# Optimization experiments

Hardware: AMD Instinct MI355X
Metric: run time of the kernel (lower is better)

## Reference

```python
import jax, jax.numpy as jnp
import numpy as np
from jax import lax

MAX_FEATURES = 50000
WIDTH = 256
EMBED = 2 * WIDTH
NUM_CLASS = 2
BATCH = 64
SEQ = 512


def setup_inputs() -> dict:
    key = jax.random.key(0)
    ks = jax.random.split(key, 10)
    s = lambda *shape: 1.0 / np.sqrt(shape[0])
    tokens = jax.random.randint(ks[0], (BATCH, SEQ), 0, MAX_FEATURES, dtype=jnp.int32)
    emb = jax.random.normal(ks[1], (MAX_FEATURES, EMBED), jnp.float32) * 0.05
    W1 = jax.random.normal(ks[2], (EMBED, WIDTH), jnp.float32) * s(EMBED)
    U1 = jax.random.normal(ks[3], (WIDTH, WIDTH), jnp.float32) * s(WIDTH)
    b1 = jnp.zeros((WIDTH,), jnp.float32)
    W2 = jax.random.normal(ks[4], (WIDTH, WIDTH), jnp.float32) * s(WIDTH)
    U2 = jax.random.normal(ks[5], (WIDTH, WIDTH), jnp.float32) * s(WIDTH)
    b2 = jnp.zeros((WIDTH,), jnp.float32)
    Wd = jax.random.normal(ks[6], (WIDTH, NUM_CLASS), jnp.float32) * s(WIDTH)
    bd = jnp.zeros((NUM_CLASS,), jnp.float32)
    return {"tokens": tokens, "emb": emb, "W1": W1, "U1": U1, "b1": b1,
            "W2": W2, "U2": U2, "b2": b2, "Wd": Wd, "bd": bd}


def _simple_rnn(x, W, U, b, return_sequences):
    # x: [B, S, D] -> precompute input projection once (big GEMM), then scan
    B = x.shape[0]
    H = U.shape[0]
    xw = jnp.einsum('bsd,dh->bsh', x, W) + b  # [B, S, H]
    def step(h, xt):
        h_new = jnp.tanh(xt + h @ U)
        return h_new, h_new
    h0 = jnp.zeros((B, H), x.dtype)
    h_last, hs = lax.scan(step, h0, jnp.swapaxes(xw, 0, 1))  # hs: [S, B, H]
    if return_sequences:
        return jnp.swapaxes(hs, 0, 1)  # [B, S, H]
    return h_last  # [B, H]


def reference(tokens, emb, W1, U1, b1, W2, U2, b2, Wd, bd):
    x = emb[tokens]                                  # [B, S, 2W] embedding lookup
    h1 = _simple_rnn(x, W1, U1, b1, return_sequences=True)   # [B, S, W]
    h2 = _simple_rnn(h1, W2, U2, b2, return_sequences=False)  # [B, W]
    logits = h2 @ Wd + bd                            # [B, num_class]
    return jax.nn.softmax(logits, axis=-1)
```

## Files before the change

### kernel.cpp

```cpp
#include <hip/hip_runtime.h>

typedef __attribute__((ext_vector_type(8))) short bf16x8;
typedef __attribute__((ext_vector_type(4))) float f32x4;

static __device__ __forceinline__ unsigned short f2bf(float x) {
    unsigned int u = __float_as_uint(x);
    u += 0x7fffu + ((u >> 16) & 1u);
    return (unsigned short)(u >> 16);
}

static __device__ __forceinline__ void barrier_lds_only() {
    __asm__ volatile("s_waitcnt lgkmcnt(0)\n\ts_barrier" ::: "memory");
}

__global__ void transpose4(const float* __restrict__ s0, const float* __restrict__ s1,
                           const float* __restrict__ s2, const float* __restrict__ s3,
                           unsigned short* __restrict__ d0, unsigned short* __restrict__ d1,
                           unsigned short* __restrict__ d2, unsigned short* __restrict__ d3) {
    int which = blockIdx.y;
    const float* src = which == 0 ? s0 : which == 1 ? s1 : which == 2 ? s2 : s3;
    unsigned short* dst = which == 0 ? d0 : which == 1 ? d1 : which == 2 ? d2 : d3;
    int K = (which == 0) ? 512 : 256;
    int idx = blockIdx.x * 256 + threadIdx.x;
    if (idx >= K * 256) return;
    int k = idx >> 8;
    int n = idx & 255;
    dst[n * K + k] = f2bf(src[idx]);
}

template<bool GATHER>
__global__ __launch_bounds__(256, 4) void gemm_mfma(
    const void* __restrict__ Aptr, const int* __restrict__ tokens,
    const unsigned short* __restrict__ Bt, const float* __restrict__ bias,
    float* __restrict__ C, int M, int N, int K)
{
    const int bn0 = blockIdx.x * 64;
    const int m0  = blockIdx.y * 64;
    const int tid = threadIdx.x;

    __shared__ unsigned short As[64 * 40];
    __shared__ unsigned short Bs[64 * 40];
    __shared__ int tok[64];

    if (GATHER) {
        if (tid < 64) tok[tid] = tokens[m0 + tid];
        __syncthreads();
    }

    const int r  = tid >> 2;
    const int c0 = (tid & 3) * 8;
    const int w  = tid >> 6;
    const int L  = tid & 63;
    const int ml = L & 15;
    const int q  = L >> 4;
    const int kq = q * 8;

    f32x4 acc[4] = {};

    for (int k0 = 0; k0 < K; k0 += 32) {
        unsigned short tmp[8];
        if (GATHER) {
            const float* src = (const float*)Aptr + (size_t)tok[r] * K + k0 + c0;
            float4 f0 = *(const float4*)(src);
            float4 f1 = *(const float4*)(src + 4);
            tmp[0]=f2bf(f0.x); tmp[1]=f2bf(f0.y); tmp[2]=f2bf(f0.z); tmp[3]=f2bf(f0.w);
            tmp[4]=f2bf(f1.x); tmp[5]=f2bf(f1.y); tmp[6]=f2bf(f1.z); tmp[7]=f2bf(f1.w);
        } else {
            const unsigned short* src = (const unsigned short*)Aptr + (size_t)(m0 + r) * K + k0 + c0;
            *(uint4*)tmp = *(const uint4*)src;
        }
        *(uint4*)&As[r * 40 + c0] = *(const uint4*)tmp;
        *(uint4*)&Bs[r * 40 + c0] = *(const uint4*)(Bt + (size_t)(bn0 + r) * K + k0 + c0);
        __syncthreads();

        bf16x8 av = *(const bf16x8*)&As[(16 * w + ml) * 40 + kq];
#pragma unroll
        for (int ns = 0; ns < 4; ++ns) {
            bf16x8 bv = *(const bf16x8*)&Bs[(ns * 16 + ml) * 40 + kq];
            acc[ns] = __builtin_amdgcn_mfma_f32_16x16x32_bf16(av, bv, acc[ns], 0, 0, 0);
        }
        __syncthreads();
    }

#pragma unroll
    for (int ns = 0; ns < 4; ++ns) {
        int gn = bn0 + ns * 16 + ml;
        float bv = bias[gn];
#pragma unroll
        for (int rr = 0; rr < 4; ++rr) {
            int gm = m0 + 16 * w + q * 4 + rr;
            C[(size_t)gm * N + gn] = acc[ns][rr] + bv;
        }
    }
}

template<bool SEQ>
__global__ __launch_bounds__(256, 1) void rnn_scan_mfma(
    const float* __restrict__ xw,
    const unsigned short* __restrict__ Ut,
    unsigned short* __restrict__ out_seq,
    float* __restrict__ out_last)
{
    const int b   = blockIdx.x;
    const int tid = threadIdx.x;
    const int w   = tid >> 6;
    const int L   = tid & 63;
    const int col = w * 64 + L;
    const int q   = L >> 4;
    const int ml  = L & 15;

    __shared__ unsigned short hsh[2][256];

    bf16x8 ufrag[4][8];
#pragma unroll
    for (int i = 0; i < 4; ++i) {
        const unsigned short* up = Ut + (size_t)((w * 4 + i) * 16 + ml) * 256 + q * 8;
#pragma unroll
        for (int kt = 0; kt < 8; ++kt)
            ufrag[i][kt] = *(const bf16x8*)(up + kt * 32);
    }

    hsh[0][tid] = 0;

    const float* xb = xw + (size_t)b * 512 * 256 + col;
    unsigned short* op = SEQ ? out_seq + (size_t)b * 512 * 256 + col : nullptr;

    float xq0 = xb[0 * 256];
    float xq1 = xb[1 * 256];
    float xq2 = xb[2 * 256];
    float xq3 = xb[3 * 256];
    const float* xpf = xb + 4 * 256;

    float lastv = 0.f;
    __syncthreads();

#define SCAN_STEP(CUR, XQ, PF)                                                       \
    {                                                                                \
        bf16x8 af[8];                                                                \
        _Pragma("unroll")                                                            \
        for (int kt = 0; kt < 8; ++kt)                                               \
            af[kt] = *(const bf16x8*)&hsh[CUR][kt * 32 + q * 8];                     \
        float xnew = 0.f;                                                            \
        if (PF) { xnew = *xpf; xpf += 256; }                                         \
        f32x4 accA[4] = {}, accB[4] = {};                                            \
        _Pragma("unroll")                                                            \
        for (int kt = 0; kt < 8; kt += 2) {                                          \
            _Pragma("unroll")                                                        \
            for (int i = 0; i < 4; ++i)                                              \
                accA[i] = __builtin_amdgcn_mfma_f32_16x16x32_bf16(af[kt], ufrag[i][kt], accA[i], 0, 0, 0);       \
            _Pragma("unroll")                                                        \
            for (int i = 0; i < 4; ++i)                                              \
                accB[i] = __builtin_amdgcn_mfma_f32_16x16x32_bf16(af[kt + 1], ufrag[i][kt + 1], accB[i], 0, 0, 0); \
        }                                                                            \
        float zA = (q == 0) ? accA[0][0] : (q == 1) ? accA[1][0] : (q == 2) ? accA[2][0] : accA[3][0]; \
        float zB = (q == 0) ? accB[0][0] : (q == 1) ? accB[1][0] : (q == 2) ? accB[2][0] : accB[3][0]; \
        float z  = zA + zB + XQ;                                                     \
        float e  = __expf(2.f * z);                  \
        float hn = 1.f - 2.f * __builtin_amdgcn_rcpf(e + 1.f);                       \
        lastv = hn;                                                                  \
        unsigned short hb = f2bf(hn);                                                \
        hsh[(CUR) ^ 1][col] = hb;                                                    \
        if (SEQ) { *op = hb; op += 256; }                                            \
        XQ = xnew;                                                                   \
        barrier_lds_only();                                                         \
    }

    for (int tt = 0; tt < 508; tt += 4) {
        SCAN_STEP(0, xq0, 1)
        SCAN_STEP(1, xq1, 1)
        SCAN_STEP(0, xq2, 1)
        SCAN_STEP(1, xq3, 1)
    }
    SCAN_STEP(0, xq0, 0)
    SCAN_STEP(1, xq1, 0)
    SCAN_STEP(0, xq2, 0)
    SCAN_STEP(1, xq3, 0)
#undef SCAN_STEP

    if (!SEQ) out_last[b * 256 + col] = lastv;
}

__global__ void head_kernel(const float* __restrict__ h2, const float* __restrict__ Wd,
                            const float* __restrict__ bd, float* __restrict__ out)
{
    int tid = threadIdx.x;
    int b = tid >> 1, c = tid & 1;
    float s = bd[c];
    for (int jj = 0; jj < 256; ++jj) s = fmaf(h2[b * 256 + jj], Wd[jj * 2 + c], s);
    __shared__ float lg[128];
    lg[tid] = s;
    __syncthreads();
    float o0 = lg[b * 2 + 0], o1 = lg[b * 2 + 1];
    float m = fmaxf(o0, o1);
    float z = __expf(o0 - m) + __expf(o1 - m);
    out[tid] = __expf(s - m) * __builtin_amdgcn_rcpf(z);
}

extern "C" void kernel_launch(void* const* d_in, const int* in_sizes, int n_in,
                              void* d_out, int out_size, void* d_ws, size_t ws_size,
                              hipStream_t stream) {
    const int*   tokens = (const int*)d_in[0];
    const float* emb    = (const float*)d_in[1];
    const float* W1     = (const float*)d_in[2];
    const float* U1     = (const float*)d_in[3];
    const float* b1     = (const float*)d_in[4];
    const float* W2     = (const float*)d_in[5];
    const float* U2     = (const float*)d_in[6];
    const float* b2     = (const float*)d_in[7];
    const float* Wd     = (const float*)d_in[8];
    const float* bd     = (const float*)d_in[9];
    float* out = (float*)d_out;

    char* ws = (char*)d_ws;
    float*          xw  = (float*)ws;
    unsigned short* h1  = (unsigned short*)(ws + (33554432));
    char*           p   = ws + 33554432 + 16777216;
    unsigned short* W1t = (unsigned short*)p;            p += 512 * 256 * 2;
    unsigned short* W2t = (unsigned short*)p;            p += 256 * 256 * 2;
    unsigned short* U1t = (unsigned short*)p;            p += 256 * 256 * 2;
    unsigned short* U2t = (unsigned short*)p;            p += 256 * 256 * 2;
    float*          h2  = (float*)p;

    const int M = 64 * 512;

    transpose4<<<dim3(512, 4), 256, 0, stream>>>(W1, W2, U1, U2, W1t, W2t, U1t, U2t);

    gemm_mfma<true><<<dim3(256 / 64, M / 64), 256, 0, stream>>>(
        emb, tokens, W1t, b1, xw, M, 256, 512);

    rnn_scan_mfma<true><<<64, 256, 0, stream>>>(xw, U1t, h1, nullptr);

    gemm_mfma<false><<<dim3(256 / 64, M / 64), 256, 0, stream>>>(
        h1, nullptr, W2t, b2, xw, M, 256, 256);

    rnn_scan_mfma<false><<<64, 256, 0, stream>>>(xw, U2t, nullptr, h2);

    head_kernel<<<1, 128, 0, stream>>>(h2, Wd, bd, out);
}
```

Baseline: 659.7 us.

## Fuse both RNN layers and second input projection into one pipelined scan kernel

Replaces the two sequential scan kernels and the middle GEMM with a single 768-thread kernel per batch row. Three warp groups play separate roles: the layer-1 recurrence, the W2 projection of h1, and the layer-2 recurrence. They are pipelined with a one-step skew through double-buffered LDS. This removes the h1 round trip through global memory, the second GEMM launch and one serial scan pass, so the two recurrences overlap in time. In exchange each block needs three times the threads and registers, the per-step work grows, and there are two extra pipeline ticks.

Result: slower. 679.2 us (+2.9%).

```diff
diff --git a/kernel.cpp b/kernel.cpp
--- a/kernel.cpp
+++ b/kernel.cpp
@@ -94,90 +94,113 @@
     }
 }
 
-template<bool SEQ>
-__global__ __launch_bounds__(256, 1) void rnn_scan_mfma(
+__global__ __launch_bounds__(768, 1) void rnn_fused(
     const float* __restrict__ xw,
-    const unsigned short* __restrict__ Ut,
-    unsigned short* __restrict__ out_seq,
+    const unsigned short* __restrict__ U1t,
+    const unsigned short* __restrict__ W2t,
+    const unsigned short* __restrict__ U2t,
+    const float* __restrict__ b2,
     float* __restrict__ out_last)
 {
-    const int b   = blockIdx.x;
-    const int tid = threadIdx.x;
-    const int w   = tid >> 6;
-    const int L   = tid & 63;
-    const int col = w * 64 + L;
-    const int q   = L >> 4;
-    const int ml  = L & 15;
-
-    __shared__ unsigned short hsh[2][256];
-
+    const int b    = blockIdx.x;
+    const int tid  = threadIdx.x;
+    const int w    = tid >> 6;
+    const int role = w >> 2;
+    const int sw   = w & 3;
+    const int L    = tid & 63;
+    const int col  = sw * 64 + L;
+    const int q    = L >> 4;
+    const int ml   = L & 15;
+
+    __shared__ unsigned short h1sh[2][256];
+    __shared__ unsigned short h2sh[2][256];
+    __shared__ float          psh[2][256];
+
+    const unsigned short* Bmat = (role == 0) ? U1t : (role == 1) ? W2t : U2t;
     bf16x8 ufrag[4][8];
 #pragma unroll
     for (int i = 0; i < 4; ++i) {
-        const unsigned short* up = Ut + (size_t)((w * 4 + i) * 16 + ml) * 256 + q * 8;
+        const unsigned short* up = Bmat + (size_t)((sw * 4 + i) * 16 + ml) * 256 + q * 8;
 #pragma unroll
         for (int kt = 0; kt < 8; ++kt)
             ufrag[i][kt] = *(const bf16x8*)(up + kt * 32);
     }
 
-    hsh[0][tid] = 0;
-
+    if (tid < 256) { h1sh[1][tid] = 0; h2sh[1][tid] = 0; }
+
+    float b2c = 0.f;
     const float* xb = xw + (size_t)b * 512 * 256 + col;
-    unsigned short* op = SEQ ? out_seq + (size_t)b * 512 * 256 + col : nullptr;
-
-    float xq0 = xb[0 * 256];
-    float xq1 = xb[1 * 256];
-    float xq2 = xb[2 * 256];
-    float xq3 = xb[3 * 256];
     const float* xpf = xb + 4 * 256;
+    float xq0 = 0.f, xq1 = 0.f, xq2 = 0.f, xq3 = 0.f;
+    if (role == 0) {
+        xq0 = xb[0 * 256]; xq1 = xb[1 * 256]; xq2 = xb[2 * 256]; xq3 = xb[3 * 256];
+    } else if (role == 2) {
+        b2c = b2[col];
+    }
 
     float lastv = 0.f;
     __syncthreads();
 
-#define SCAN_STEP(CUR, XQ, PF)                                                       \
+#define LADDER(SRCBUF, RP)                                                           \
+    bf16x8 af[8];                                                                    \
+    _Pragma("unroll")                                                                \
+    for (int kt = 0; kt < 8; ++kt)                                                   \
+        af[kt] = *(const bf16x8*)&SRCBUF[RP][kt * 32 + q * 8];                       \
+    f32x4 acc[4] = {};                                                               \
+    _Pragma("unroll")                                                                \
+    for (int kt = 0; kt < 8; ++kt) {                                                 \
+        _Pragma("unroll")                                                            \
+        for (int i = 0; i < 4; ++i)                                                  \
+            acc[i] = __builtin_amdgcn_mfma_f32_16x16x32_bf16(af[kt], ufrag[i][kt], acc[i], 0, 0, 0); \
+    }                                                                                \
+    float z = (q == 0) ? acc[0][0] : (q == 1) ? acc[1][0] : (q == 2) ? acc[2][0] : acc[3][0];
+
+#define TICK(RP, XQ, PF, DO_A, DO_B, DO_C)                                           \
     {                                                                                \
-        bf16x8 af[8];                                                                \
-        _Pragma("unroll")                                                            \
-        for (int kt = 0; kt < 8; ++kt)                                               \
-            af[kt] = *(const bf16x8*)&hsh[CUR][kt * 32 + q * 8];                     \
-        float xnew = 0.f;                                                            \
-        if (PF) { xnew = *xpf; xpf += 256; }                                         \
-        f32x4 accA[4] = {}, accB[4] = {};                                            \
-        _Pragma("unroll")                                                            \
-        for (int kt = 0; kt < 8; kt += 2) {                                          \
-            _Pragma("unroll")                                                        \
-            for (int i = 0; i < 4; ++i)                                              \
-                accA[i] = __builtin_amdgcn_mfma_f32_16x16x32_bf16(af[kt], ufrag[i][kt], accA[i], 0, 0, 0);       \
-            _Pragma("unroll")                                                        \
-            for (int i = 0; i < 4; ++i)                                              \
-                accB[i] = __builtin_amdgcn_mfma_f32_16x16x32_bf16(af[kt + 1], ufrag[i][kt + 1], accB[i], 0, 0, 0); \
+        if (DO_A && role == 0) {                                                     \
+            float xnew = 0.f;                                                        \
+            if (PF) { xnew = *xpf; xpf += 256; }                                     \
+            LADDER(h1sh, RP)                                                         \
+            z += XQ;                                                                 \
+            float e  = __expf(2.f * z);              \
+            float hn = 1.f - 2.f * __builtin_amdgcn_rcpf(e + 1.f);                   \
+            h1sh[(RP) ^ 1][col] = f2bf(hn);                                          \
+            XQ = xnew;                                                               \
+        } else if (DO_B && role == 1) {                                              \
+            LADDER(h1sh, RP)                                                         \
+            psh[(RP) ^ 1][col] = z;                                                  \
+        } else if (DO_C && role == 2) {                                              \
+            float pv = psh[RP][col] + b2c;                                           \
+            LADDER(h2sh, RP)                                                         \
+            z += pv;                                                                 \
+            float e  = __expf(2.f * z);                                              \
+            float hn = 1.f - 2.f * __builtin_amdgcn_rcpf(e + 1.f);                   \
+            lastv = hn;                                                              \
+            h2sh[(RP) ^ 1][col] = f2bf(hn);                                          \
         }                                                                            \
-        float zA = (q == 0) ? accA[0][0] : (q == 1) ? accA[1][0] : (q == 2) ? accA[2][0] : accA[3][0]; \
-        float zB = (q == 0) ? accB[0][0] : (q == 1) ? accB[1][0] : (q == 2) ? accB[2][0] : accB[3][0]; \
-        float z  = zA + zB + XQ;                                                     \
-        float e  = __expf(2.f * z);                  \
-        float hn = 1.f - 2.f * __builtin_amdgcn_rcpf(e + 1.f);                       \
-        lastv = hn;                                                                  \
-        unsigned short hb = f2bf(hn);                                                \
-        hsh[(CUR) ^ 1][col] = hb;                                                    \
-        if (SEQ) { *op = hb; op += 256; }                                            \
-        XQ = xnew;                                                                   \
-        barrier_lds_only();                                                         \
-    }
-
-    for (int tt = 0; tt < 508; tt += 4) {
-        SCAN_STEP(0, xq0, 1)
-        SCAN_STEP(1, xq1, 1)
-        SCAN_STEP(0, xq2, 1)
-        SCAN_STEP(1, xq3, 1)
-    }
-    SCAN_STEP(0, xq0, 0)
-    SCAN_STEP(1, xq1, 0)
-    SCAN_STEP(0, xq2, 0)
-    SCAN_STEP(1, xq3, 0)
-#undef SCAN_STEP
-
-    if (!SEQ) out_last[b * 256 + col] = lastv;
+        barrier_lds_only();                                                          \
+    }
+
+    TICK(1, xq0, 1, 1, 1, 0)
+    TICK(0, xq1, 1, 1, 1, 0)
+    TICK(1, xq2, 1, 1, 1, 1)
+    TICK(0, xq3, 1, 1, 1, 1)
+    for (int tt = 4; tt < 508; tt += 4) {
+        TICK(1, xq0, 1, 1, 1, 1)
+        TICK(0, xq1, 1, 1, 1, 1)
+        TICK(1, xq2, 1, 1, 1, 1)
+        TICK(0, xq3, 1, 1, 1, 1)
+    }
+    TICK(1, xq0, 0, 1, 1, 1)
+    TICK(0, xq1, 0, 1, 1, 1)
+    TICK(1, xq2, 0, 1, 1, 1)
+    TICK(0, xq3, 0, 1, 1, 1)
+    TICK(1, xq0, 0, 0, 1, 1)
+    TICK(0, xq0, 0, 0, 0, 1)
+#undef TICK
+#undef LADDER
+
+    if (role == 2) out_last[b * 256 + col] = lastv;
 }
 
 __global__ void head_kernel(const float* __restrict__ h2, const float* __restrict__ Wd,
@@ -213,7 +236,6 @@
 
     char* ws = (char*)d_ws;
     float*          xw  = (float*)ws;
-    unsigned short* h1  = (unsigned short*)(ws + (33554432));
     char*           p   = ws + 33554432 + 16777216;
     unsigned short* W1t = (unsigned short*)p;            p += 512 * 256 * 2;
     unsigned short* W2t = (unsigned short*)p;            p += 256 * 256 * 2;
@@ -228,12 +250,7 @@
     gemm_mfma<true><<<dim3(256 / 64, M / 64), 256, 0, stream>>>(
         emb, tokens, W1t, b1, xw, M, 256, 512);
 
-    rnn_scan_mfma<true><<<64, 256, 0, stream>>>(xw, U1t, h1, nullptr);
-
-    gemm_mfma<false><<<dim3(256 / 64, M / 64), 256, 0, stream>>>(
-        h1, nullptr, W2t, b2, xw, M, 256, 256);
-
-    rnn_scan_mfma<false><<<64, 256, 0, stream>>>(xw, U2t, nullptr, h2);
+    rnn_fused<<<64, 768, 0, stream>>>(xw, U1t, W2t, U2t, b2, h2);
 
     head_kernel<<<1, 128, 0, stream>>>(h2, Wd, bd, out);
 }
```

## Fuse layer-2 input projection into layer-1 scan, drop intermediate h1 GEMM

Applied to the files above, without the earlier changes.

The first recurrent scan now also keeps W2 fragments in registers and multiplies each step's previous hidden state by W2. It writes the layer-2 pre-activation (plus b2) in place into the xw buffer one step behind, so the bf16 h1 sequence is never stored and the separate layer-2 GEMM launch is removed. The MFMA chains are also split into more independent accumulators to shorten dependency latency. This doubles the MFMA work and register pressure on the serial critical path of the first scan, in exchange for removing a full GEMM and its memory traffic.

New measurement: 983.2 us. 49.0% more time.

```diff
diff --git a/kernel.cpp b/kernel.cpp
--- a/kernel.cpp
+++ b/kernel.cpp
@@ -94,90 +94,194 @@
     }
 }
 
-template<bool SEQ>
-__global__ __launch_bounds__(256, 1) void rnn_scan_mfma(
+__global__ __launch_bounds__(256, 1) void rnn_scan_fused(
+    float* __restrict__ xw,
+    const unsigned short* __restrict__ U1t,
+    const unsigned short* __restrict__ W2t,
+    const float* __restrict__ b2)
+{
+    const int b   = blockIdx.x;
+    const int tid = threadIdx.x;
+    const int w   = tid >> 6;
+    const int L   = tid & 63;
+    const int col = tid;
+    const int q   = L >> 4;
+    const int ml  = L & 15;
+
+    __shared__ unsigned short hsh[2][256];
+
+    bf16x8 U1f[4][8], W2f[4][8];
+#pragma unroll
+    for (int i = 0; i < 4; ++i) {
+        const unsigned short* u1 = U1t + (size_t)((w * 4 + i) * 16 + ml) * 256 + q * 8;
+        const unsigned short* w2 = W2t + (size_t)((w * 4 + i) * 16 + ml) * 256 + q * 8;
+#pragma unroll
+        for (int kt = 0; kt < 8; ++kt) {
+            U1f[i][kt] = *(const bf16x8*)(u1 + kt * 32);
+            W2f[i][kt] = *(const bf16x8*)(w2 + kt * 32);
+        }
+    }
+
+    hsh[0][tid] = 0;
+    const float b2c = b2[col];
+    float* xb        = xw + (size_t)b * 512 * 256 + col;
+    const float* xpf = xb + 4 * 256;
+    float* pst       = xb - 256;
+    float xq0 = xb[0 * 256], xq1 = xb[1 * 256], xq2 = xb[2 * 256], xq3 = xb[3 * 256];
+    const f32x4 z4 = {0.f, 0.f, 0.f, 0.f};
+    __syncthreads();
+
+#define FTICK(RP, XQ, PF, ST)                                                        \
+    {                                                                                \
+        bf16x8 af[8];                                                                \
+        _Pragma("unroll")                                                            \
+        for (int kt = 0; kt < 8; ++kt)                                               \
+            af[kt] = *(const bf16x8*)&hsh[RP][kt * 32 + q * 8];                      \
+        float xnew = 0.f;                                                            \
+        if (PF) { xnew = *xpf; xpf += 256; }                                         \
+        f32x4 aU[4][4];                                                              \
+        f32x4 aW[4][2];                                                              \
+        _Pragma("unroll")                                                            \
+        for (int kt = 0; kt < 8; ++kt) {                                             \
+            _Pragma("unroll")                                                        \
+            for (int i = 0; i < 4; ++i)                                              \
+                aU[i][kt & 3] = __builtin_amdgcn_mfma_f32_16x16x32_bf16(             \
+                    af[kt], U1f[i][kt], (kt < 4) ? z4 : aU[i][kt & 3], 0, 0, 0);     \
+            _Pragma("unroll")                                                        \
+            for (int i = 0; i < 4; ++i)                                              \
+                aW[i][kt & 1] = __builtin_amdgcn_mfma_f32_16x16x32_bf16(             \
+                    af[kt], W2f[i][kt], (kt < 2) ? z4 : aW[i][kt & 1], 0, 0, 0);     \
+        }                                                                            \
+        float sU0 = aU[0][0][0] + aU[0][1][0] + aU[0][2][0] + aU[0][3][0];           \
+        float sU1 = aU[1][0][0] + aU[1][1][0] + aU[1][2][0] + aU[1][3][0];           \
+        float sU2 = aU[2][0][0] + aU[2][1][0] + aU[2][2][0] + aU[2][3][0];           \
+        float sU3 = aU[3][0][0] + aU[3][1][0] + aU[3][2][0] + aU[3][3][0];           \
+        float z = ((q == 0) ? sU0 : (q == 1) ? sU1 : (q == 2) ? sU2 : sU3) + XQ;     \
+        float e  = __expf(2.f * z);                  \
+        float hn = 1.f - 2.f * __builtin_amdgcn_rcpf(e + 1.f);                       \
+        hsh[(RP) ^ 1][col] = f2bf(hn);                                               \
+        if (ST) {                                                                    \
+            float sW0 = aW[0][0][0] + aW[0][1][0];                                   \
+            float sW1 = aW[1][0][0] + aW[1][1][0];                                   \
+            float sW2 = aW[2][0][0] + aW[2][1][0];                                   \
+            float sW3 = aW[3][0][0] + aW[3][1][0];                                   \
+            *pst = ((q == 0) ? sW0 : (q == 1) ? sW1 : (q == 2) ? sW2 : sW3) + b2c;   \
+        }                                                                            \
+        pst += 256;                                                                  \
+        XQ = xnew;                                                                   \
+        barrier_lds_only();                                                          \
+    }
+
+    FTICK(0, xq0, 1, 0)
+    FTICK(1, xq1, 1, 1)
+    FTICK(0, xq2, 1, 1)
+    FTICK(1, xq3, 1, 1)
+    for (int tt = 4; tt < 508; tt += 4) {
+        FTICK(0, xq0, 1, 1)
+        FTICK(1, xq1, 1, 1)
+        FTICK(0, xq2, 1, 1)
+        FTICK(1, xq3, 1, 1)
+    }
+    FTICK(0, xq0, 0, 1)
+    FTICK(1, xq1, 0, 1)
+    FTICK(0, xq2, 0, 1)
+    FTICK(1, xq3, 0, 1)
+#undef FTICK
+
+    {
+        bf16x8 af[8];
+#pragma unroll
+        for (int kt = 0; kt < 8; ++kt)
+            af[kt] = *(const bf16x8*)&hsh[0][kt * 32 + q * 8];
+        f32x4 aW[4][2];
+#pragma unroll
+        for (int kt = 0; kt < 8; ++kt)
+#pragma unroll
+            for (int i = 0; i < 4; ++i)
+                aW[i][kt & 1] = __builtin_amdgcn_mfma_f32_16x16x32_bf16(
+                    af[kt], W2f[i][kt], (kt < 2) ? z4 : aW[i][kt & 1], 0, 0, 0);
+        float sW0 = aW[0][0][0] + aW[0][1][0];
+        float sW1 = aW[1][0][0] + aW[1][1][0];
+        float sW2 = aW[2][0][0] + aW[2][1][0];
+        float sW3 = aW[3][0][0] + aW[3][1][0];
+        *pst = ((q == 0) ? sW0 : (q == 1) ? sW1 : (q == 2) ? sW2 : sW3) + b2c;
+    }
+}
+
+__global__ __launch_bounds__(256, 1) void rnn_scan2(
     const float* __restrict__ xw,
     const unsigned short* __restrict__ Ut,
-    unsigned short* __restrict__ out_seq,
     float* __restrict__ out_last)
 {
     const int b   = blockIdx.x;
     const int tid = threadIdx.x;
     const int w   = tid >> 6;
     const int L   = tid & 63;
-    const int col = w * 64 + L;
+    const int col = tid;
     const int q   = L >> 4;
     const int ml  = L & 15;
 
     __shared__ unsigned short hsh[2][256];
 
-    bf16x8 ufrag[4][8];
+    bf16x8 uf[4][8];
 #pragma unroll
     for (int i = 0; i < 4; ++i) {
         const unsigned short* up = Ut + (size_t)((w * 4 + i) * 16 + ml) * 256 + q * 8;
 #pragma unroll
         for (int kt = 0; kt < 8; ++kt)
-            ufrag[i][kt] = *(const bf16x8*)(up + kt * 32);
+            uf[kt == 0 ? i : i][kt] = *(const bf16x8*)(up + kt * 32);
     }
 
     hsh[0][tid] = 0;
-
-    const float* xb = xw + (size_t)b * 512 * 256 + col;
-    unsigned short* op = SEQ ? out_seq + (size_t)b * 512 * 256 + col : nullptr;
-
-    float xq0 = xb[0 * 256];
-    float xq1 = xb[1 * 256];
-    float xq2 = xb[2 * 256];
-    float xq3 = xb[3 * 256];
+    const float* xb  = xw + (size_t)b * 512 * 256 + col;
     const float* xpf = xb + 4 * 256;
-
+    float xq0 = xb[0 * 256], xq1 = xb[1 * 256], xq2 = xb[2 * 256], xq3 = xb[3 * 256];
+    const f32x4 z4 = {0.f, 0.f, 0.f, 0.f};
     float lastv = 0.f;
     __syncthreads();
 
-#define SCAN_STEP(CUR, XQ, PF)                                                       \
+#define STICK(RP, XQ, PF)                                                            \
     {                                                                                \
         bf16x8 af[8];                                                                \
         _Pragma("unroll")                                                            \
         for (int kt = 0; kt < 8; ++kt)                                               \
-            af[kt] = *(const bf16x8*)&hsh[CUR][kt * 32 + q * 8];                     \
+            af[kt] = *(const bf16x8*)&hsh[RP][kt * 32 + q * 8];                      \
         float xnew = 0.f;                                                            \
         if (PF) { xnew = *xpf; xpf += 256; }                                         \
-        f32x4 accA[4] = {}, accB[4] = {};                                            \
+        f32x4 aU[4][4];                                                              \
         _Pragma("unroll")                                                            \
-        for (int kt = 0; kt < 8; kt += 2) {                                          \
+        for (int kt = 0; kt < 8; ++kt) {                                             \
             _Pragma("unroll")                                                        \
             for (int i = 0; i < 4; ++i)                                              \
-                accA[i] = __builtin_amdgcn_mfma_f32_16x16x32_bf16(af[kt], ufrag[i][kt], accA[i], 0, 0, 0);       \
-            _Pragma("unroll")                                                        \
-            for (int i = 0; i < 4; ++i)                                              \
-                accB[i] = __builtin_amdgcn_mfma_f32_16x16x32_bf16(af[kt + 1], ufrag[i][kt + 1], accB[i], 0, 0, 0); \
+                aU[i][kt & 3] = __builtin_amdgcn_mfma_f32_16x16x32_bf16(             \
+                    af[kt], uf[i][kt], (kt < 4) ? z4 : aU[i][kt & 3], 0, 0, 0);      \
         }                                                                            \
-        float zA = (q == 0) ? accA[0][0] : (q == 1) ? accA[1][0] : (q == 2) ? accA[2][0] : accA[3][0]; \
-        float zB = (q == 0) ? accB[0][0] : (q == 1) ? accB[1][0] : (q == 2) ? accB[2][0] : accB[3][0]; \
-        float z  = zA + zB + XQ;                                                     \
-        float e  = __expf(2.f * z);                  \
+        float s0 = aU[0][0][0] + aU[0][1][0] + aU[0][2][0] + aU[0][3][0];            \
+        float s1 = aU[1][0][0] + aU[1][1][0] + aU[1][2][0] + aU[1][3][0];            \
+        float s2 = aU[2][0][0] + aU[2][1][0] + aU[2][2][0] + aU[2][3][0];            \
+        float s3 = aU[3][0][0] + aU[3][1][0] + aU[3][2][0] + aU[3][3][0];            \
+        float z = ((q == 0) ? s0 : (q == 1) ? s1 : (q == 2) ? s2 : s3) + XQ;         \
+        float e  = __expf(2.f * z);                                                  \
         float hn = 1.f - 2.f * __builtin_amdgcn_rcpf(e + 1.f);                       \
         lastv = hn;                                                                  \
-        unsigned short hb = f2bf(hn);                                                \
-        hsh[(CUR) ^ 1][col] = hb;                                                    \
-        if (SEQ) { *op = hb; op += 256; }                                            \
+        hsh[(RP) ^ 1][col] = f2bf(hn);                                               \
         XQ = xnew;                                                                   \
-        barrier_lds_only();                                                         \
+        barrier_lds_only();                                                          \
     }
 
     for (int tt = 0; tt < 508; tt += 4) {
-        SCAN_STEP(0, xq0, 1)
-        SCAN_STEP(1, xq1, 1)
-        SCAN_STEP(0, xq2, 1)
-        SCAN_STEP(1, xq3, 1)
-    }
-    SCAN_STEP(0, xq0, 0)
-    SCAN_STEP(1, xq1, 0)
-    SCAN_STEP(0, xq2, 0)
-    SCAN_STEP(1, xq3, 0)
-#undef SCAN_STEP
-
-    if (!SEQ) out_last[b * 256 + col] = lastv;
+        STICK(0, xq0, 1)
+        STICK(1, xq1, 1)
+        STICK(0, xq2, 1)
+        STICK(1, xq3, 1)
+    }
+    STICK(0, xq0, 0)
+    STICK(1, xq1, 0)
+    STICK(0, xq2, 0)
+    STICK(1, xq3, 0)
+#undef STICK
+
+    out_last[b * 256 + col] = lastv;
 }
 
 __global__ void head_kernel(const float* __restrict__ h2, const float* __restrict__ Wd,
@@ -213,7 +317,6 @@
 
     char* ws = (char*)d_ws;
     float*          xw  = (float*)ws;
-    unsigned short* h1  = (unsigned short*)(ws + (33554432));
     char*           p   = ws + 33554432 + 16777216;
     unsigned short* W1t = (unsigned short*)p;            p += 512 * 256 * 2;
     unsigned short* W2t = (unsigned short*)p;            p += 256 * 256 * 2;
@@ -228,12 +331,9 @@
     gemm_mfma<true><<<dim3(256 / 64, M / 64), 256, 0, stream>>>(
         emb, tokens, W1t, b1, xw, M, 256, 512);
 
-    rnn_scan_mfma<true><<<64, 256, 0, stream>>>(xw, U1t, h1, nullptr);
-
-    gemm_mfma<false><<<dim3(256 / 64, M / 64), 256, 0, stream>>>(
-        h1, nullptr, W2t, b2, xw, M, 256, 256);
-
-    rnn_scan_mfma<false><<<64, 256, 0, stream>>>(xw, U2t, nullptr, h2);
+    rnn_scan_fused<<<64, 256, 0, stream>>>(xw, U1t, W2t, b2);
+
+    rnn_scan2<<<64, 256, 0, stream>>>(xw, U2t, h2);
 
     head_kernel<<<1, 128, 0, stream>>>(h2, Wd, bd, out);
 }
```

## Pipeline both RNN layers in one kernel with flag-based producer-consumer sync

Applied to the files above, without the earlier changes.

Merges the layer-1 scan, the layer-2 input GEMM and the layer-2 scan into one 128-block kernel. Blocks 0-63 run layer 1 and publish h1 in chunks of 8 steps through release flags. Blocks 64-127 poll those flags and compute the W2 input projection inline alongside the U2 recurrence. This removes one scan launch and the separate GEMM, and overlaps the two sequential scans instead of running them back to back. In exchange it relies on all 128 blocks being co-resident, and the spin-wait uses a bounded timeout that silently breaks out, which could read stale h1 data.

Result: slower. 878.3 us (+33.1%).

```diff
diff --git a/kernel.cpp b/kernel.cpp
--- a/kernel.cpp
+++ b/kernel.cpp
@@ -7,6 +7,10 @@
     unsigned int u = __float_as_uint(x);
     u += 0x7fffu + ((u >> 16) & 1u);
     return (unsigned short)(u >> 16);
+}
+
+static __device__ __forceinline__ float selq(const f32x4* a, int q) {
+    return (q == 0) ? a[0][0] : (q == 1) ? a[1][0] : (q == 2) ? a[2][0] : a[3][0];
 }
 
 static __device__ __forceinline__ void barrier_lds_only() {
@@ -94,47 +98,47 @@
     }
 }
 
-template<bool SEQ>
-__global__ __launch_bounds__(256, 1) void rnn_scan_mfma(
+__global__ __launch_bounds__(256, 1) void rnn_pipe(
     const float* __restrict__ xw,
-    const unsigned short* __restrict__ Ut,
-    unsigned short* __restrict__ out_seq,
+    const unsigned short* __restrict__ U1t,
+    const unsigned short* __restrict__ W2t,
+    const unsigned short* __restrict__ U2t,
+    const float* __restrict__ b2,
+    unsigned short* h1g,
+    int* flags,
     float* __restrict__ out_last)
 {
-    const int b   = blockIdx.x;
+    const int bid = blockIdx.x;
     const int tid = threadIdx.x;
     const int w   = tid >> 6;
     const int L   = tid & 63;
-    const int col = w * 64 + L;
+    const int col = tid;
     const int q   = L >> 4;
     const int ml  = L & 15;
 
     __shared__ unsigned short hsh[2][256];
 
-    bf16x8 ufrag[4][8];
-#pragma unroll
-    for (int i = 0; i < 4; ++i) {
-        const unsigned short* up = Ut + (size_t)((w * 4 + i) * 16 + ml) * 256 + q * 8;
-#pragma unroll
-        for (int kt = 0; kt < 8; ++kt)
-            ufrag[i][kt] = *(const bf16x8*)(up + kt * 32);
-    }
-
-    hsh[0][tid] = 0;
-
-    const float* xb = xw + (size_t)b * 512 * 256 + col;
-    unsigned short* op = SEQ ? out_seq + (size_t)b * 512 * 256 + col : nullptr;
-
-    float xq0 = xb[0 * 256];
-    float xq1 = xb[1 * 256];
-    float xq2 = xb[2 * 256];
-    float xq3 = xb[3 * 256];
-    const float* xpf = xb + 4 * 256;
-
-    float lastv = 0.f;
-    __syncthreads();
-
-#define SCAN_STEP(CUR, XQ, PF)                                                       \
+    if (bid < 64) {
+        const int b = bid;
+        int* flagp = flags + b;
+
+        bf16x8 U1f[4][8];
+#pragma unroll
+        for (int i = 0; i < 4; ++i) {
+            const unsigned short* up = U1t + (size_t)((w * 4 + i) * 16 + ml) * 256 + q * 8;
+#pragma unroll
+            for (int kt = 0; kt < 8; ++kt)
+                U1f[i][kt] = *(const bf16x8*)(up + kt * 32);
+        }
+        hsh[0][tid] = 0;
+
+        const float* xb  = xw + (size_t)b * 512 * 256 + col;
+        const float* xpf = xb + 4 * 256;
+        unsigned short* op = h1g + (((size_t)b * 512) << 8) + col;
+        float xq0 = xb[0 * 256], xq1 = xb[1 * 256], xq2 = xb[2 * 256], xq3 = xb[3 * 256];
+        __syncthreads();
+
+#define PSTEP(CUR, XQ, PF)                                                           \
     {                                                                                \
         bf16x8 af[8];                                                                \
         _Pragma("unroll")                                                            \
@@ -147,37 +151,123 @@
         for (int kt = 0; kt < 8; kt += 2) {                                          \
             _Pragma("unroll")                                                        \
             for (int i = 0; i < 4; ++i)                                              \
-                accA[i] = __builtin_amdgcn_mfma_f32_16x16x32_bf16(af[kt], ufrag[i][kt], accA[i], 0, 0, 0);       \
-            _Pragma("unroll")                                                        \
-            for (int i = 0; i < 4; ++i)                                              \
-                accB[i] = __builtin_amdgcn_mfma_f32_16x16x32_bf16(af[kt + 1], ufrag[i][kt + 1], accB[i], 0, 0, 0); \
+                accA[i] = __builtin_amdgcn_mfma_f32_16x16x32_bf16(af[kt], U1f[i][kt], accA[i], 0, 0, 0);       \
+            _Pragma("unroll")                                                        \
+            for (int i = 0; i < 4; ++i)                                              \
+                accB[i] = __builtin_amdgcn_mfma_f32_16x16x32_bf16(af[kt + 1], U1f[i][kt + 1], accB[i], 0, 0, 0); \
         }                                                                            \
-        float zA = (q == 0) ? accA[0][0] : (q == 1) ? accA[1][0] : (q == 2) ? accA[2][0] : accA[3][0]; \
-        float zB = (q == 0) ? accB[0][0] : (q == 1) ? accB[1][0] : (q == 2) ? accB[2][0] : accB[3][0]; \
-        float z  = zA + zB + XQ;                                                     \
+        float z  = selq(accA, q) + selq(accB, q) + XQ;                               \
         float e  = __expf(2.f * z);                  \
         float hn = 1.f - 2.f * __builtin_amdgcn_rcpf(e + 1.f);                       \
-        lastv = hn;                                                                  \
         unsigned short hb = f2bf(hn);                                                \
         hsh[(CUR) ^ 1][col] = hb;                                                    \
-        if (SEQ) { *op = hb; op += 256; }                                            \
+        *op = hb; op += 256;                                                         \
         XQ = xnew;                                                                   \
-        barrier_lds_only();                                                         \
-    }
-
-    for (int tt = 0; tt < 508; tt += 4) {
-        SCAN_STEP(0, xq0, 1)
-        SCAN_STEP(1, xq1, 1)
-        SCAN_STEP(0, xq2, 1)
-        SCAN_STEP(1, xq3, 1)
-    }
-    SCAN_STEP(0, xq0, 0)
-    SCAN_STEP(1, xq1, 0)
-    SCAN_STEP(0, xq2, 0)
-    SCAN_STEP(1, xq3, 0)
-#undef SCAN_STEP
-
-    if (!SEQ) out_last[b * 256 + col] = lastv;
+        barrier_lds_only();                                                          \
+    }
+
+        for (int g = 0; g < 63; ++g) {
+            PSTEP(0, xq0, 1) PSTEP(1, xq1, 1) PSTEP(0, xq2, 1) PSTEP(1, xq3, 1)
+            PSTEP(0, xq0, 1) PSTEP(1, xq1, 1) PSTEP(0, xq2, 1) PSTEP(1, xq3, 1)
+            asm volatile("s_waitcnt vmcnt(0)" ::: "memory");
+            __builtin_amdgcn_s_barrier();
+            if (tid == 0)
+                __hip_atomic_store(flagp, 8 * g + 8, __ATOMIC_RELEASE, __HIP_MEMORY_SCOPE_AGENT);
+        }
+        PSTEP(0, xq0, 1) PSTEP(1, xq1, 1) PSTEP(0, xq2, 1) PSTEP(1, xq3, 1)
+        PSTEP(0, xq0, 0) PSTEP(1, xq1, 0) PSTEP(0, xq2, 0) PSTEP(1, xq3, 0)
+#undef PSTEP
+        asm volatile("s_waitcnt vmcnt(0)" ::: "memory");
+        __builtin_amdgcn_s_barrier();
+        if (tid == 0)
+            __hip_atomic_store(flagp, 512, __ATOMIC_RELEASE, __HIP_MEMORY_SCOPE_AGENT);
+    } else {
+        const int b = bid - 64;
+        int* flagp = flags + b;
+
+        bf16x8 U2f[4][8], W2f[4][8];
+#pragma unroll
+        for (int i = 0; i < 4; ++i) {
+            const unsigned short* u2 = U2t + (size_t)((w * 4 + i) * 16 + ml) * 256 + q * 8;
+            const unsigned short* w2 = W2t + (size_t)((w * 4 + i) * 16 + ml) * 256 + q * 8;
+#pragma unroll
+            for (int kt = 0; kt < 8; ++kt) {
+                U2f[i][kt] = *(const bf16x8*)(u2 + kt * 32);
+                W2f[i][kt] = *(const bf16x8*)(w2 + kt * 32);
+            }
+        }
+        const float b2c = b2[col];
+        hsh[0][tid] = 0;
+        const unsigned short* h1b = h1g + (((size_t)b * 512) << 8) + q * 8;
+        float lastv = 0.f;
+        bf16x8 hA[8], hB[8];
+        __syncthreads();
+
+#define LOADH(BUF, T)                                                                \
+    {                                                                                \
+        const unsigned short* hr = h1b + (((size_t)(T)) << 8);                       \
+        _Pragma("unroll")                                                            \
+        for (int kt = 0; kt < 8; ++kt)                                               \
+            BUF[kt] = *(const bf16x8*)(hr + kt * 32);                                \
+    }
+
+#define CSTEP(RP, BUF, PT)                                                           \
+    {                                                                                \
+        bf16x8 af[8];                                                                \
+        _Pragma("unroll")                                                            \
+        for (int kt = 0; kt < 8; ++kt)                                               \
+            af[kt] = *(const bf16x8*)&hsh[RP][kt * 32 + q * 8];                     \
+        f32x4 aA[4] = {}, aB[4] = {}, wA[4] = {}, wB[4] = {};                        \
+        _Pragma("unroll")                                                            \
+        for (int kt = 0; kt < 8; kt += 2) {                                          \
+            _Pragma("unroll")                                                        \
+            for (int i = 0; i < 4; ++i)                                              \
+                wA[i] = __builtin_amdgcn_mfma_f32_16x16x32_bf16(BUF[kt], W2f[i][kt], wA[i], 0, 0, 0);          \
+            _Pragma("unroll")                                                        \
+            for (int i = 0; i < 4; ++i)                                              \
+                aA[i] = __builtin_amdgcn_mfma_f32_16x16x32_bf16(af[kt], U2f[i][kt], aA[i], 0, 0, 0);           \
+            _Pragma("unroll")                                                        \
+            for (int i = 0; i < 4; ++i)                                              \
+                wB[i] = __builtin_amdgcn_mfma_f32_16x16x32_bf16(BUF[kt + 1], W2f[i][kt + 1], wB[i], 0, 0, 0);  \
+            _Pragma("unroll")                                                        \
+            for (int i = 0; i < 4; ++i)                                              \
+                aB[i] = __builtin_amdgcn_mfma_f32_16x16x32_bf16(af[kt + 1], U2f[i][kt + 1], aB[i], 0, 0, 0);   \
+        }                                                                            \
+        float z  = selq(aA, q) + selq(aB, q) + selq(wA, q) + selq(wB, q) + b2c;      \
+        float e  = __expf(2.f * z);                                                  \
+        float hn = 1.f - 2.f * __builtin_amdgcn_rcpf(e + 1.f);                       \
+        lastv = hn;                                                                  \
+        hsh[(RP) ^ 1][col] = f2bf(hn);                                               \
+        if ((PT) >= 0) LOADH(BUF, PT)                                                \
+        barrier_lds_only();                                                          \
+    }
+
+        for (int g = 0; g < 64; ++g) {
+            const int t0 = 8 * g;
+            if (tid == 0) {
+                int it = 0;
+                while (__hip_atomic_load(flagp, __ATOMIC_ACQUIRE, __HIP_MEMORY_SCOPE_AGENT) < t0 + 8) {
+                    __builtin_amdgcn_s_sleep(2);
+                    if (++it > (1 << 17)) break;
+                }
+            }
+            __syncthreads();
+            LOADH(hA, t0 + 0)
+            LOADH(hB, t0 + 1)
+            CSTEP(0, hA, t0 + 2)
+            CSTEP(1, hB, t0 + 3)
+            CSTEP(0, hA, t0 + 4)
+            CSTEP(1, hB, t0 + 5)
+            CSTEP(0, hA, t0 + 6)
+            CSTEP(1, hB, t0 + 7)
+            CSTEP(0, hA, -1)
+            CSTEP(1, hB, -1)
+        }
+#undef CSTEP
+#undef LOADH
+
+        out_last[b * 256 + col] = lastv;
+    }
 }
 
 __global__ void head_kernel(const float* __restrict__ h2, const float* __restrict__ Wd,
@@ -213,27 +303,25 @@
 
     char* ws = (char*)d_ws;
     float*          xw  = (float*)ws;
-    unsigned short* h1  = (unsigned short*)(ws + (33554432));
+    unsigned short* h1g = (unsigned short*)(ws + 33554432);
     char*           p   = ws + 33554432 + 16777216;
     unsigned short* W1t = (unsigned short*)p;            p += 512 * 256 * 2;
     unsigned short* W2t = (unsigned short*)p;            p += 256 * 256 * 2;
     unsigned short* U1t = (unsigned short*)p;            p += 256 * 256 * 2;
     unsigned short* U2t = (unsigned short*)p;            p += 256 * 256 * 2;
-    float*          h2  = (float*)p;
+    float*          h2  = (float*)p;                     p += 64 * 256 * 4;
+    int*            flags = (int*)p;
 
     const int M = 64 * 512;
+
+    hipMemsetAsync(flags, 0, 64 * sizeof(int), stream);
 
     transpose4<<<dim3(512, 4), 256, 0, stream>>>(W1, W2, U1, U2, W1t, W2t, U1t, U2t);
 
     gemm_mfma<true><<<dim3(256 / 64, M / 64), 256, 0, stream>>>(
         emb, tokens, W1t, b1, xw, M, 256, 512);
 
-    rnn_scan_mfma<true><<<64, 256, 0, stream>>>(xw, U1t, h1, nullptr);
-
-    gemm_mfma<false><<<dim3(256 / 64, M / 64), 256, 0, stream>>>(
-        h1, nullptr, W2t, b2, xw, M, 256, 256);
-
-    rnn_scan_mfma<false><<<64, 256, 0, stream>>>(xw, U2t, nullptr, h2);
+    rnn_pipe<<<128, 256, 0, stream>>>(xw, U1t, W2t, U2t, b2, h1g, flags, h2);
 
     head_kernel<<<1, 128, 0, stream>>>(h2, Wd, bd, out);
 }
```
